# Performance work log

Measured on AMD Instinct MI355X. Metric: run time of the kernel, lower is better.

## Reference

```python
import jax, jax.numpy as jnp
import numpy as np

EPS = 1e-5

def conv2x2(x, w, b):
    # x: NCHW, w: OIHW (2x2), stride 2, valid padding
    y = jax.lax.conv_general_dilated(x, w, window_strides=(2, 2), padding='VALID',
                                     dimension_numbers=('NCHW', 'OIHW', 'NCHW'))
    return y + b[None, :, None, None]

def instancenorm(x):
    # per-sample, per-channel norm over H,W; biased variance, no affine (PyTorch defaults)
    mu = jnp.mean(x, axis=(2, 3), keepdims=True)
    var = jnp.mean(jnp.square(x - mu), axis=(2, 3), keepdims=True)
    return (x - mu) * jax.lax.rsqrt(var + EPS)

def lrelu(x):
    return jax.nn.leaky_relu(x, negative_slope=0.01)

def setup_inputs() -> dict:
    key = jax.random.key(0)
    ks = jax.random.split(key, 14)
    B, L = 256, 20
    s = 0.05
    inp = {
        'x': jax.random.normal(ks[0], (B, 3, 128, 128), jnp.float32),
        'labels': jax.random.uniform(ks[1], (B, L), jnp.float32),
        'w1': jax.random.normal(ks[2], (16, 3, 2, 2), jnp.float32) * s,
        'b1': jnp.zeros((16,), jnp.float32),
        'w2': jax.random.normal(ks[3], (32, 16 + L, 2, 2), jnp.float32) * s,
        'b2': jnp.zeros((32,), jnp.float32),
        'w3': jax.random.normal(ks[4], (64, 32, 2, 2), jnp.float32) * s,
        'b3': jnp.zeros((64,), jnp.float32),
        'w4': jax.random.normal(ks[5], (128, 64, 2, 2), jnp.float32) * s,
        'b4': jnp.zeros((128,), jnp.float32),
        'fcw1': jax.random.normal(ks[6], (1024, 128 * 8 * 8), jnp.float32) * s,
        'fcb1': jnp.zeros((1024,), jnp.float32),
        'fcw2': jax.random.normal(ks[7], (1, 1024), jnp.float32) * s,
        'fcb2': jnp.zeros((1,), jnp.float32),
    }
    return inp

def reference(x, labels, w1, b1, w2, b2, w3, b3, w4, b4, fcw1, fcb1, fcw2, fcb2):
    h = lrelu(instancenorm(conv2x2(x, w1, b1)))            # [B,16,64,64]
    # vectorized replacement of the per-element label broadcast loop
    lab = jnp.broadcast_to(labels[:, :, None, None],
                           (h.shape[0], labels.shape[1], h.shape[2], h.shape[3]))
    h = jnp.concatenate([h, lab], axis=1)                  # [B,36,64,64]
    h = lrelu(instancenorm(conv2x2(h, w2, b2)))            # [B,32,32,32]
    h = lrelu(instancenorm(conv2x2(h, w3, b3)))            # [B,64,16,16]
    h = lrelu(instancenorm(conv2x2(h, w4, b4)))            # [B,128,8,8]
    h = h.reshape(h.shape[0], -1)                          # [B,8192]
    h = lrelu(h @ fcw1.T + fcb1)                           # [B,1024]
    return h @ fcw2.T + fcb2                               # [B,1]
```

## Files before the change

### kernel.cpp

```cpp
#include <hip/hip_runtime.h>

#define EPSI 1e-5f

typedef __attribute__((ext_vector_type(8))) short bf16x8;
typedef __attribute__((ext_vector_type(4))) float f32x4;

__device__ __forceinline__ float lrelu(float x) { return x > 0.f ? x : 0.01f * x; }

__device__ __forceinline__ unsigned short f2bf(float x) {
    unsigned int u = __float_as_uint(x);
    return (unsigned short)((u + 0x7fffu + ((u >> 16) & 1u)) >> 16);
}
__device__ __forceinline__ unsigned int pack2(float a, float b) {
    return (unsigned int)f2bf(a) | ((unsigned int)f2bf(b) << 16);
}
__device__ __forceinline__ bf16x8 pack8(float4 a, float4 b) {
    union { unsigned short u[8]; bf16x8 v; } p;
    p.u[0] = f2bf(a.x); p.u[1] = f2bf(a.y); p.u[2] = f2bf(a.z); p.u[3] = f2bf(a.w);
    p.u[4] = f2bf(b.x); p.u[5] = f2bf(b.y); p.u[6] = f2bf(b.z); p.u[7] = f2bf(b.w);
    return p.v;
}

__device__ __forceinline__ float2 block_reduce_sum2(float a, float b) {
    #pragma unroll
    for (int off = 1; off < 64; off <<= 1) {
        a += __shfl_xor(a, off, 64);
        b += __shfl_xor(b, off, 64);
    }
    __shared__ float lds[8];
    const int t = threadIdx.x;
    if ((t & 63) == 0) { lds[2 * (t >> 6)] = a; lds[2 * (t >> 6) + 1] = b; }
    __syncthreads();
    a = lds[0] + lds[2] + lds[4] + lds[6];
    b = lds[1] + lds[3] + lds[5] + lds[7];
    return make_float2(a, b);
}


__global__ __launch_bounds__(1024) void wprep(const float* __restrict__ w2,
                                              const float* __restrict__ w3,
                                              const float* __restrict__ w4,
                                              unsigned short* __restrict__ wk) {
    const int g = blockIdx.x * 1024 + threadIdx.x;
    if (g < 2048) {
        const int co = g >> 6, k = g & 63;
        const int ic = (k >> 4) * 4 + (k & 3), row = (k >> 3) & 1, tx = (k >> 2) & 1;
        wk[g] = f2bf(w2[co * 144 + ic * 4 + row * 2 + tx]);
    } else if (g < 10240) {
        const int e = g - 2048, co = e >> 7, k = e & 127;
        const int ic = (k >> 4) * 4 + (k & 3), row = (k >> 3) & 1, tx = (k >> 2) & 1;
        wk[g] = f2bf(w3[co * 128 + ic * 4 + row * 2 + tx]);
    } else if (g < 43008) {
        const int e = g - 10240, co = e >> 8, k = e & 255;
        const int ic = (k >> 4) * 4 + (k & 3), row = (k >> 3) & 1, tx = (k >> 2) & 1;
        wk[g] = f2bf(w4[co * 256 + ic * 4 + row * 2 + tx]);
    }
}

__global__ __launch_bounds__(1024, 1) void k1_conv_in(const float* __restrict__ x,
                                                      const float* __restrict__ w1,
                                                      unsigned short* __restrict__ h1) {
    const int n = blockIdx.x;
    const int t = threadIdx.x;
    __shared__ float red[16][16][2];
    __shared__ float msc[16][2];
    const float* xn = x + (size_t)n * 49152;
    float acc[16][4];
    #pragma unroll
    for (int j = 0; j < 16; ++j)
        #pragma unroll
        for (int q = 0; q < 4; ++q) acc[j][q] = 0.f;
    #pragma unroll 1
    for (int ic = 0; ic < 3; ++ic) {
        const float* p = xn + ic * 16384;
        float2 v0[4], v1[4];
        #pragma unroll
        for (int q = 0; q < 4; ++q) {
            const int idx = t + 1024 * q;
            const int oy = idx >> 6, ox = idx & 63;
            v0[q] = ((const float2*)(p + (2 * oy) * 128))[ox];
            v1[q] = ((const float2*)(p + (2 * oy + 1) * 128))[ox];
        }
        #pragma unroll
        for (int j = 0; j < 16; ++j) {
            const float4 wv = *(const float4*)(w1 + j * 12 + ic * 4);
            #pragma unroll
            for (int q = 0; q < 4; ++q)
                acc[j][q] += v0[q].x * wv.x + v0[q].y * wv.y + v1[q].x * wv.z + v1[q].y * wv.w;
        }
    }
    const int w = t >> 6, l = t & 63;
    #pragma unroll
    for (int j = 0; j < 16; ++j) {
        float s1 = acc[j][0] + acc[j][1] + acc[j][2] + acc[j][3];
        float s2 = acc[j][0] * acc[j][0] + acc[j][1] * acc[j][1] +
                   acc[j][2] * acc[j][2] + acc[j][3] * acc[j][3];
        #pragma unroll
        for (int off = 1; off < 64; off <<= 1) {
            s1 += __shfl_xor(s1, off, 64);
            s2 += __shfl_xor(s2, off, 64);
        }
        if (l == 0) { red[w][j][0] = s1; red[w][j][1] = s2; }
    }
    __syncthreads();
    if (t < 16) {
        float s1 = 0.f, s2 = 0.f;
        #pragma unroll
        for (int ww = 0; ww < 16; ++ww) { s1 += red[ww][t][0]; s2 += red[ww][t][1]; }
        const float mean = s1 * (1.f / 4096.f);
        const float var = s2 * (1.f / 4096.f) - mean * mean;
        msc[t][0] = mean; msc[t][1] = rsqrtf(var + EPSI);
    }
    __syncthreads();
    unsigned short* on = h1 + (size_t)n * 65536;
    #pragma unroll
    for (int q = 0; q < 4; ++q) {
        const int px = t + 1024 * q;
        #pragma unroll
        for (int q4 = 0; q4 < 4; ++q4) {
            const float n0 = lrelu((acc[4 * q4 + 0][q] - msc[4 * q4 + 0][0]) * msc[4 * q4 + 0][1]);
            const float n1 = lrelu((acc[4 * q4 + 1][q] - msc[4 * q4 + 1][0]) * msc[4 * q4 + 1][1]);
            const float n2 = lrelu((acc[4 * q4 + 2][q] - msc[4 * q4 + 2][0]) * msc[4 * q4 + 2][1]);
            const float n3 = lrelu((acc[4 * q4 + 3][q] - msc[4 * q4 + 3][0]) * msc[4 * q4 + 3][1]);
            uint2 u; u.x = pack2(n0, n1); u.y = pack2(n2, n3);
            *(uint2*)(on + ((size_t)q4 * 4096 + px) * 4) = u;
        }
    }
}

__global__ __launch_bounds__(1024, 1) void k234(const unsigned short* __restrict__ h1,
                                                const unsigned short* __restrict__ wk,
                                                unsigned short* __restrict__ h4) {
    const int n = blockIdx.x;
    const int t = threadIdx.x;
    const int w = t >> 6, l = t & 63;
    __shared__ unsigned short h2s[32768];
    __shared__ unsigned short h3s[16384];
    __shared__ float ps[4][64][32];
    __shared__ float red[16][64][2];
    __shared__ float msc[64][2];
    const unsigned short* h1n = h1 + (size_t)n * 65536;

    {
        const unsigned short* wk2 = wk;
        bf16x8 af[2][2];
        #pragma unroll
        for (int cf = 0; cf < 2; ++cf)
            #pragma unroll
            for (int ks = 0; ks < 2; ++ks)
                af[cf][ks] = *(const bf16x8*)(wk2 + (cf * 16 + (l & 15)) * 64 + ks * 32 + (l >> 4) * 8);
        f32x4 acc[4][2];
        const f32x4 z = {0.f, 0.f, 0.f, 0.f};
        #pragma unroll
        for (int pg = 0; pg < 4; ++pg) { acc[pg][0] = z; acc[pg][1] = z; }
        const int row = (l >> 4) & 1, icq0 = (l >> 4) >> 1;
        #pragma unroll
        for (int pg = 0; pg < 4; ++pg) {
            const int oy = 2 * w + (pg >> 1);
            const int ox = (pg & 1) * 16 + (l & 15);
            #pragma unroll
            for (int ks = 0; ks < 2; ++ks) {
                const bf16x8 bv = *(const bf16x8*)(h1n + (ks * 2 + icq0) * 16384 + (2 * oy + row) * 256 + ox * 8);
                acc[pg][0] = __builtin_amdgcn_mfma_f32_16x16x32_bf16(af[0][ks], bv, acc[pg][0], 0, 0, 0);
                acc[pg][1] = __builtin_amdgcn_mfma_f32_16x16x32_bf16(af[1][ks], bv, acc[pg][1], 0, 0, 0);
            }
        }
        #pragma unroll
        for (int cf = 0; cf < 2; ++cf) {
            #pragma unroll
            for (int r = 0; r < 4; ++r) {
                float s1 = acc[0][cf][r] + acc[1][cf][r] + acc[2][cf][r] + acc[3][cf][r];
                float s2 = acc[0][cf][r] * acc[0][cf][r] + acc[1][cf][r] * acc[1][cf][r] +
                           acc[2][cf][r] * acc[2][cf][r] + acc[3][cf][r] * acc[3][cf][r];
                #pragma unroll
                for (int off = 1; off < 16; off <<= 1) {
                    s1 += __shfl_xor(s1, off, 64);
                    s2 += __shfl_xor(s2, off, 64);
                }
                if ((l & 15) == 0) {
                    red[w][cf * 16 + (l >> 4) * 4 + r][0] = s1;
                    red[w][cf * 16 + (l >> 4) * 4 + r][1] = s2;
                }
            }
        }
        __syncthreads();
        if (t < 32) {
            float s1 = 0.f, s2 = 0.f;
            #pragma unroll
            for (int ww = 0; ww < 16; ++ww) { s1 += red[ww][t][0]; s2 += red[ww][t][1]; }
            const float mean = s1 * (1.f / 1024.f);
            const float var = s2 * (1.f / 1024.f) - mean * mean;
            msc[t][0] = mean; msc[t][1] = rsqrtf(var + EPSI);
        }
        __syncthreads();
        #pragma unroll
        for (int pg = 0; pg < 4; ++pg) {
            const int px = w * 64 + pg * 16 + (l & 15);
            #pragma unroll
            for (int cf = 0; cf < 2; ++cf) {
                const int co0 = cf * 16 + (l >> 4) * 4;
                float v[4];
                #pragma unroll
                for (int r = 0; r < 4; ++r)
                    v[r] = lrelu((acc[pg][cf][r] - msc[co0 + r][0]) * msc[co0 + r][1]);
                uint2 u; u.x = pack2(v[0], v[1]); u.y = pack2(v[2], v[3]);
                *(uint2*)(&h2s[((cf * 4 + (l >> 4)) * 1024 + px) * 4]) = u;
            }
        }
    }
    __syncthreads();

    {
        const unsigned short* wk3 = wk + 2048;
        f32x4 acc[4];
        const f32x4 z = {0.f, 0.f, 0.f, 0.f};
        #pragma unroll
        for (int cf = 0; cf < 4; ++cf) acc[cf] = z;
        const int row = (l >> 4) & 1, icq0 = (l >> 4) >> 1;
        #pragma unroll
        for (int ks = 0; ks < 4; ++ks) {
            const bf16x8 bv = *(const bf16x8*)(&h2s[(ks * 2 + icq0) * 4096 + (2 * w + row) * 128 + (l & 15) * 8]);
            #pragma unroll
            for (int cf = 0; cf < 4; ++cf) {
                const bf16x8 af = *(const bf16x8*)(wk3 + (cf * 16 + (l & 15)) * 128 + ks * 32 + (l >> 4) * 8);
                acc[cf] = __builtin_amdgcn_mfma_f32_16x16x32_bf16(af, bv, acc[cf], 0, 0, 0);
            }
        }
        #pragma unroll
        for (int cf = 0; cf < 4; ++cf) {
            #pragma unroll
            for (int r = 0; r < 4; ++r) {
                float s1 = acc[cf][r], s2 = acc[cf][r] * acc[cf][r];
                #pragma unroll
                for (int off = 1; off < 16; off <<= 1) {
                    s1 += __shfl_xor(s1, off, 64);
                    s2 += __shfl_xor(s2, off, 64);
                }
                if ((l & 15) == 0) {
                    red[w][cf * 16 + (l >> 4) * 4 + r][0] = s1;
                    red[w][cf * 16 + (l >> 4) * 4 + r][1] = s2;
                }
            }
        }
        __syncthreads();
        if (t < 64) {
            float s1 = 0.f, s2 = 0.f;
            #pragma unroll
            for (int ww = 0; ww < 16; ++ww) { s1 += red[ww][t][0]; s2 += red[ww][t][1]; }
            const float mean = s1 * (1.f / 256.f);
            const float var = s2 * (1.f / 256.f) - mean * mean;
            msc[t][0] = mean; msc[t][1] = rsqrtf(var + EPSI);
        }
        __syncthreads();
        const int px = w * 16 + (l & 15);
        #pragma unroll
        for (int cf = 0; cf < 4; ++cf) {
            const int co0 = cf * 16 + (l >> 4) * 4;
            float v[4];
            #pragma unroll
            for (int r = 0; r < 4; ++r)
                v[r] = lrelu((acc[cf][r] - msc[co0 + r][0]) * msc[co0 + r][1]);
            uint2 u; u.x = pack2(v[0], v[1]); u.y = pack2(v[2], v[3]);
            *(uint2*)(&h3s[((cf * 4 + (l >> 4)) * 256 + px) * 4]) = u;
        }
    }
    __syncthreads();

    {
        const unsigned short* wk4 = wk + 10240;
        const int cfp = w & 3, khalf = (w >> 2) & 1;
        f32x4 acc[4][2];
        const f32x4 z = {0.f, 0.f, 0.f, 0.f};
        #pragma unroll
        for (int pg = 0; pg < 4; ++pg) { acc[pg][0] = z; acc[pg][1] = z; }
        const int row = (l >> 4) & 1, icq0 = (l >> 4) >> 1;
        const int oyb = (l & 15) >> 3, ox = l & 7;
        if (w < 8) {
            #pragma unroll
            for (int ksl = 0; ksl < 4; ++ksl) {
                const int ks = khalf * 4 + ksl;
                bf16x8 af0 = *(const bf16x8*)(wk4 + ((cfp * 2 + 0) * 16 + (l & 15)) * 256 + ks * 32 + (l >> 4) * 8);
                bf16x8 af1 = *(const bf16x8*)(wk4 + ((cfp * 2 + 1) * 16 + (l & 15)) * 256 + ks * 32 + (l >> 4) * 8);
                #pragma unroll
                for (int pg = 0; pg < 4; ++pg) {
                    const int oy = pg * 2 + oyb;
                    const bf16x8 bv = *(const bf16x8*)(&h3s[(ks * 2 + icq0) * 1024 + (2 * oy + row) * 64 + ox * 8]);
                    acc[pg][0] = __builtin_amdgcn_mfma_f32_16x16x32_bf16(af0, bv, acc[pg][0], 0, 0, 0);
                    acc[pg][1] = __builtin_amdgcn_mfma_f32_16x16x32_bf16(af1, bv, acc[pg][1], 0, 0, 0);
                }
            }
        }
        if (w < 4) {
            #pragma unroll
            for (int pg = 0; pg < 4; ++pg)
                #pragma unroll
                for (int cfi = 0; cfi < 2; ++cfi)
                    #pragma unroll
                    for (int r = 0; r < 4; ++r)
                        ps[cfp][l][pg * 8 + cfi * 4 + r] = acc[pg][cfi][r];
        }
        __syncthreads();
        if (w >= 4 && w < 8) {
            unsigned short* on = h4 + (size_t)n * 8192;
            #pragma unroll
            for (int cfi = 0; cfi < 2; ++cfi) {
                #pragma unroll
                for (int r = 0; r < 4; ++r) {
                    float v[4];
                    #pragma unroll
                    for (int pg = 0; pg < 4; ++pg)
                        v[pg] = acc[pg][cfi][r] + ps[cfp][l][pg * 8 + cfi * 4 + r];
                    float s1 = v[0] + v[1] + v[2] + v[3];
                    float s2 = v[0] * v[0] + v[1] * v[1] + v[2] * v[2] + v[3] * v[3];
                    #pragma unroll
                    for (int off = 1; off < 16; off <<= 1) {
                        s1 += __shfl_xor(s1, off, 64);
                        s2 += __shfl_xor(s2, off, 64);
                    }
                    const float mean = s1 * (1.f / 64.f);
                    const float var = s2 * (1.f / 64.f) - mean * mean;
                    const float sc = rsqrtf(var + EPSI);
                    const int co = (cfp * 2 + cfi) * 16 + (l >> 4) * 4 + r;
                    #pragma unroll
                    for (int pg = 0; pg < 4; ++pg)
                        on[co * 64 + pg * 16 + (l & 15)] = f2bf(lrelu((v[pg] - mean) * sc));
                }
            }
        }
    }
}

__global__ __launch_bounds__(256, 2) void k5_fc1(const unsigned short* __restrict__ A,
                                                 const float* __restrict__ Wf,
                                                 float* __restrict__ Cp) {
    __shared__ unsigned short As[128 * 72];
    __shared__ unsigned short Bs[128 * 72];
    const int t = threadIdx.x;
    const int sk = blockIdx.x >> 4;
    const int tile = blockIdx.x & 15;
    const int mt = tile >> 3, nt = tile & 7;
    const int m0 = mt * 128, n0 = nt * 128;
    const int w = t >> 6, l = t & 63;
    const int wm = (w >> 1) * 64, wn = (w & 1) * 64;
    const int lr16 = l & 15, lk8 = (l >> 4) * 8;
    const int srow = t >> 3, scol = (t & 7) * 8;
    f32x4 acc[4][4];
    const f32x4 z = {0.f, 0.f, 0.f, 0.f};
    #pragma unroll
    for (int f = 0; f < 4; ++f)
        #pragma unroll
        for (int g = 0; g < 4; ++g) acc[f][g] = z;
    const int kbeg = sk * 512;
    #pragma unroll 1
    for (int kt = 0; kt < 8; ++kt) {
        const int kc = kbeg + kt * 64;
        bf16x8 av[4], bv[4];
        #pragma unroll
        for (int i = 0; i < 4; ++i) {
            av[i] = *(const bf16x8*)(A + (size_t)(m0 + srow + 32 * i) * 8192 + kc + scol);
            const float4 w0 = *(const float4*)(Wf + (size_t)(n0 + srow + 32 * i) * 8192 + kc + scol);
            const float4 w1 = *(const float4*)(Wf + (size_t)(n0 + srow + 32 * i) * 8192 + kc + scol + 4);
            bv[i] = pack8(w0, w1);
        }
        __syncthreads();
        #pragma unroll
        for (int i = 0; i < 4; ++i) {
            *(bf16x8*)&As[(srow + 32 * i) * 72 + scol] = av[i];
            *(bf16x8*)&Bs[(srow + 32 * i) * 72 + scol] = bv[i];
        }
        __syncthreads();
        #pragma unroll
        for (int ks = 0; ks < 2; ++ks) {
            bf16x8 af[4], bfr[4];
            #pragma unroll
            for (int f = 0; f < 4; ++f)
                af[f] = *(const bf16x8*)&As[(wm + f * 16 + lr16) * 72 + ks * 32 + lk8];
            #pragma unroll
            for (int g = 0; g < 4; ++g)
                bfr[g] = *(const bf16x8*)&Bs[(wn + g * 16 + lr16) * 72 + ks * 32 + lk8];
            #pragma unroll
            for (int f = 0; f < 4; ++f)
                #pragma unroll
                for (int g = 0; g < 4; ++g)
                    acc[f][g] = __builtin_amdgcn_mfma_f32_16x16x32_bf16(af[f], bfr[g], acc[f][g], 0, 0, 0);
        }
    }
    const int orow = (l >> 4) * 4, ocol = l & 15;
    #pragma unroll
    for (int f = 0; f < 4; ++f) {
        #pragma unroll
        for (int g = 0; g < 4; ++g) {
            #pragma unroll
            for (int j = 0; j < 4; ++j) {
                const int m = m0 + wm + f * 16 + orow + j;
                const int nn = n0 + wn + g * 16 + ocol;
                Cp[((size_t)sk * 256 + m) * 1024 + nn] = acc[f][g][j];
            }
        }
    }
}

__global__ __launch_bounds__(256) void k6_fc2(const float* __restrict__ Cp,
                                              const float* __restrict__ bias,
                                              const float* __restrict__ w,
                                              const float* __restrict__ b,
                                              float* __restrict__ out) {
    const int n = blockIdx.x, t = threadIdx.x;
    float part = 0.f;
    #pragma unroll
    for (int i = 0; i < 4; ++i) {
        const int nn = t + 256 * i;
        float s = 0.f;
        #pragma unroll
        for (int sk = 0; sk < 16; ++sk)
            s += Cp[((size_t)sk * 256 + n) * 1024 + nn];
        part += lrelu(s + bias[nn]) * w[nn];
    }
    const float2 red = block_reduce_sum2(part, 0.f);
    if (t == 0) out[n] = red.x + b[0];
}

extern "C" void kernel_launch(void* const* d_in, const int* in_sizes, int n_in,
                              void* d_out, int out_size, void* d_ws, size_t ws_size,
                              hipStream_t stream) {
    (void)in_sizes; (void)n_in; (void)out_size; (void)ws_size;
    const float* x    = (const float*)d_in[0];
    const float* w1   = (const float*)d_in[2];
    const float* w2   = (const float*)d_in[4];
    const float* w3   = (const float*)d_in[6];
    const float* w4   = (const float*)d_in[8];
    const float* fcw1 = (const float*)d_in[10];
    const float* fcb1 = (const float*)d_in[11];
    const float* fcw2 = (const float*)d_in[12];
    const float* fcb2 = (const float*)d_in[13];
    float* out = (float*)d_out;
    float* bufA = (float*)d_ws;
    float* bufB = bufA + 16777216;
    unsigned short* h1 = (unsigned short*)bufA;
    unsigned short* h4 = (unsigned short*)bufB;
    unsigned short* wk = (unsigned short*)bufB + 12582912;
    float* Cp = bufA;
    wprep<<<42, 1024, 0, stream>>>(w2, w3, w4, wk);
    k1_conv_in<<<256, 1024, 0, stream>>>(x, w1, h1);
    k234<<<256, 1024, 0, stream>>>(h1, wk, h4);
    k5_fc1<<<256, 256, 0, stream>>>(h4, fcw1, Cp);
    k6_fc2<<<256, 256, 0, stream>>>(Cp, fcb1, fcw2, fcb2, out);
}
```

Before: 83.86 us.

## Fold weight prep into conv1, double FC1 split-K, store partials in bf16

Merges the weight-conversion kernel into the first conv kernel, so the first 42 blocks also convert w2-w4 to bf16, and one launch disappears. FC1 split-K goes from 16 to 32 slices (512 blocks) to fill more CUs. Partial sums are now written as bf16 to halve that traffic, and FC2 reads them vectorised. Rounding partials to bf16 before the reduction adds numerical error.

```diff
diff --git a/kernel.cpp b/kernel.cpp
--- a/kernel.cpp
+++ b/kernel.cpp
@@ -11,6 +11,8 @@
     unsigned int u = __float_as_uint(x);
     return (unsigned short)((u + 0x7fffu + ((u >> 16) & 1u)) >> 16);
 }
+__device__ __forceinline__ float bflo(unsigned int v) { return __uint_as_float(v << 16); }
+__device__ __forceinline__ float bfhi(unsigned int v) { return __uint_as_float(v & 0xFFFF0000u); }
 __device__ __forceinline__ unsigned int pack2(float a, float b) {
     return (unsigned int)f2bf(a) | ((unsigned int)f2bf(b) << 16);
 }
@@ -37,31 +39,31 @@
 }
 
 
-__global__ __launch_bounds__(1024) void wprep(const float* __restrict__ w2,
-                                              const float* __restrict__ w3,
-                                              const float* __restrict__ w4,
-                                              unsigned short* __restrict__ wk) {
-    const int g = blockIdx.x * 1024 + threadIdx.x;
-    if (g < 2048) {
-        const int co = g >> 6, k = g & 63;
-        const int ic = (k >> 4) * 4 + (k & 3), row = (k >> 3) & 1, tx = (k >> 2) & 1;
-        wk[g] = f2bf(w2[co * 144 + ic * 4 + row * 2 + tx]);
-    } else if (g < 10240) {
-        const int e = g - 2048, co = e >> 7, k = e & 127;
-        const int ic = (k >> 4) * 4 + (k & 3), row = (k >> 3) & 1, tx = (k >> 2) & 1;
-        wk[g] = f2bf(w3[co * 128 + ic * 4 + row * 2 + tx]);
-    } else if (g < 43008) {
-        const int e = g - 10240, co = e >> 8, k = e & 255;
-        const int ic = (k >> 4) * 4 + (k & 3), row = (k >> 3) & 1, tx = (k >> 2) & 1;
-        wk[g] = f2bf(w4[co * 256 + ic * 4 + row * 2 + tx]);
-    }
-}
-
 __global__ __launch_bounds__(1024, 1) void k1_conv_in(const float* __restrict__ x,
                                                       const float* __restrict__ w1,
-                                                      unsigned short* __restrict__ h1) {
+                                                      const float* __restrict__ w2,
+                                                      const float* __restrict__ w3,
+                                                      const float* __restrict__ w4,
+                                                      unsigned short* __restrict__ h1,
+                                                      unsigned short* __restrict__ wk) {
     const int n = blockIdx.x;
     const int t = threadIdx.x;
+    if (n < 42) {
+        const int g = n * 1024 + t;
+        if (g < 2048) {
+            const int co = g >> 6, k = g & 63;
+            const int ic = (k >> 4) * 4 + (k & 3), row = (k >> 3) & 1, tx = (k >> 2) & 1;
+            wk[g] = f2bf(w2[co * 144 + ic * 4 + row * 2 + tx]);
+        } else if (g < 10240) {
+            const int e = g - 2048, co = e >> 7, k = e & 127;
+            const int ic = (k >> 4) * 4 + (k & 3), row = (k >> 3) & 1, tx = (k >> 2) & 1;
+            wk[g] = f2bf(w3[co * 128 + ic * 4 + row * 2 + tx]);
+        } else if (g < 43008) {
+            const int e = g - 10240, co = e >> 8, k = e & 255;
+            const int ic = (k >> 4) * 4 + (k & 3), row = (k >> 3) & 1, tx = (k >> 2) & 1;
+            wk[g] = f2bf(w4[co * 256 + ic * 4 + row * 2 + tx]);
+        }
+    }
     __shared__ float red[16][16][2];
     __shared__ float msc[16][2];
     const float* xn = x + (size_t)n * 49152;
@@ -332,7 +334,7 @@
 
 __global__ __launch_bounds__(256, 2) void k5_fc1(const unsigned short* __restrict__ A,
                                                  const float* __restrict__ Wf,
-                                                 float* __restrict__ Cp) {
+                                                 unsigned short* __restrict__ Cp) {
     __shared__ unsigned short As[128 * 72];
     __shared__ unsigned short Bs[128 * 72];
     const int t = threadIdx.x;
@@ -350,9 +352,9 @@
     for (int f = 0; f < 4; ++f)
         #pragma unroll
         for (int g = 0; g < 4; ++g) acc[f][g] = z;
-    const int kbeg = sk * 512;
+    const int kbeg = sk * 256;
     #pragma unroll 1
-    for (int kt = 0; kt < 8; ++kt) {
+    for (int kt = 0; kt < 4; ++kt) {
         const int kc = kbeg + kt * 64;
         bf16x8 av[4], bv[4];
         #pragma unroll
@@ -394,28 +396,29 @@
             for (int j = 0; j < 4; ++j) {
                 const int m = m0 + wm + f * 16 + orow + j;
                 const int nn = n0 + wn + g * 16 + ocol;
-                Cp[((size_t)sk * 256 + m) * 1024 + nn] = acc[f][g][j];
-            }
-        }
-    }
-}
-
-__global__ __launch_bounds__(256) void k6_fc2(const float* __restrict__ Cp,
+                Cp[((size_t)sk * 256 + m) * 1024 + nn] = f2bf(acc[f][g][j]);
+            }
+        }
+    }
+}
+
+__global__ __launch_bounds__(256) void k6_fc2(const unsigned short* __restrict__ Cp,
                                               const float* __restrict__ bias,
                                               const float* __restrict__ w,
                                               const float* __restrict__ b,
                                               float* __restrict__ out) {
     const int n = blockIdx.x, t = threadIdx.x;
-    float part = 0.f;
-    #pragma unroll
-    for (int i = 0; i < 4; ++i) {
-        const int nn = t + 256 * i;
-        float s = 0.f;
-        #pragma unroll
-        for (int sk = 0; sk < 16; ++sk)
-            s += Cp[((size_t)sk * 256 + n) * 1024 + nn];
-        part += lrelu(s + bias[nn]) * w[nn];
-    }
+    const int nn0 = t * 4;
+    float s0 = 0.f, s1 = 0.f, s2 = 0.f, s3 = 0.f;
+    #pragma unroll
+    for (int sk = 0; sk < 32; ++sk) {
+        const uint2 u = *(const uint2*)(Cp + ((size_t)sk * 256 + n) * 1024 + nn0);
+        s0 += bflo(u.x); s1 += bfhi(u.x); s2 += bflo(u.y); s3 += bfhi(u.y);
+    }
+    const float4 bi = *(const float4*)(bias + nn0);
+    const float4 wv = *(const float4*)(w + nn0);
+    float part = lrelu(s0 + bi.x) * wv.x + lrelu(s1 + bi.y) * wv.y +
+                 lrelu(s2 + bi.z) * wv.z + lrelu(s3 + bi.w) * wv.w;
     const float2 red = block_reduce_sum2(part, 0.f);
     if (t == 0) out[n] = red.x + b[0];
 }
@@ -439,10 +442,9 @@
     unsigned short* h1 = (unsigned short*)bufA;
     unsigned short* h4 = (unsigned short*)bufB;
     unsigned short* wk = (unsigned short*)bufB + 12582912;
-    float* Cp = bufA;
-    wprep<<<42, 1024, 0, stream>>>(w2, w3, w4, wk);
-    k1_conv_in<<<256, 1024, 0, stream>>>(x, w1, h1);
+    unsigned short* Cp = (unsigned short*)bufA;
+    k1_conv_in<<<256, 1024, 0, stream>>>(x, w1, w2, w3, w4, h1, wk);
     k234<<<256, 1024, 0, stream>>>(h1, wk, h4);
-    k5_fc1<<<256, 256, 0, stream>>>(h4, fcw1, Cp);
+    k5_fc1<<<512, 256, 0, stream>>>(h4, fcw1, Cp);
     k6_fc2<<<256, 256, 0, stream>>>(Cp, fcb1, fcw2, fcb2, out);
 }
```

New measurement: 76.52 us. 8.8% less time.
